# Kernel optimization log

Hardware: AMD Instinct MI355X
Metric: run time of the kernel (lower is better)

The kernel has to match this reference:

```python
import jax, jax.numpy as jnp
import numpy as np

FEAT_RES = 512
FEAT_DIM = 48
WIDTH = 128
IN_DIM = FEAT_DIM + 27 + 63  # 138
N_RAYS, N_SAMPLES = 4096, 128


def positional_encode(x, L):
    freqs = (2.0 ** jnp.arange(L)).astype(x.dtype)            # [L]
    xf = x[..., None, :] * freqs[:, None]                      # [..., L, 3]
    enc = jnp.concatenate([jnp.sin(xf), jnp.cos(xf)], axis=-1) # [..., L, 6]
    return jnp.concatenate([x, enc.reshape(x.shape[:-1] + (L * 6,))], axis=-1)


def grid_sample_bilinear(plane, gx, gy):
    # plane: [C, H, W]; gx, gy: [N, S] in [-1, 1]; align_corners=True, zeros padding
    H, W = plane.shape[-2], plane.shape[-1]
    ix = (gx + 1.0) * 0.5 * (W - 1)
    iy = (gy + 1.0) * 0.5 * (H - 1)
    x0 = jnp.floor(ix); y0 = jnp.floor(iy)
    x1 = x0 + 1.0;      y1 = y0 + 1.0
    wx1 = ix - x0; wx0 = 1.0 - wx1
    wy1 = iy - y0; wy0 = 1.0 - wy1

    def gather(xi, yi, w):
        valid = (xi >= 0) & (xi <= W - 1) & (yi >= 0) & (yi <= H - 1)
        xc = jnp.clip(xi, 0, W - 1).astype(jnp.int32)
        yc = jnp.clip(yi, 0, H - 1).astype(jnp.int32)
        v = plane[:, yc, xc]                                   # [C, N, S]
        return v * (w * valid.astype(w.dtype))[None]

    return (gather(x0, y0, wx0 * wy0) + gather(x1, y0, wx1 * wy0)
            + gather(x0, y1, wx0 * wy1) + gather(x1, y1, wx1 * wy1))


def setup_inputs() -> dict:
    key = jax.random.key(0)
    ks = jax.random.split(key, 12)
    x = jax.random.uniform(ks[0], (N_RAYS, N_SAMPLES, 3), jnp.float32, -3.0, 3.0)
    d = jax.random.normal(ks[1], (N_RAYS, 3), jnp.float32)
    d = d / jnp.linalg.norm(d, axis=-1, keepdims=True)
    feat = jax.random.normal(ks[2], (3, FEAT_DIM, FEAT_RES, FEAT_RES), jnp.float32)
    s = 0.05
    W0 = jax.random.normal(ks[3], (IN_DIM, WIDTH), jnp.float32) * s
    b0 = jnp.zeros((WIDTH,), jnp.float32)
    W1 = jax.random.normal(ks[4], (WIDTH, WIDTH), jnp.float32) * s
    b1 = jnp.zeros((WIDTH,), jnp.float32)
    W2 = jax.random.normal(ks[5], (WIDTH, WIDTH), jnp.float32) * s
    b2 = jnp.zeros((WIDTH,), jnp.float32)
    W3 = jax.random.normal(ks[6], (WIDTH, 4), jnp.float32) * s
    b3 = jnp.zeros((4,), jnp.float32)
    return {"x": x, "d": d, "feat": feat, "W0": W0, "b0": b0,
            "W1": W1, "b1": b1, "W2": W2, "b2": b2, "W3": W3, "b3": b3}


def reference(x, d, feat, W0, b0, W1, b1, W2, b2, W3, b3):
    x = x / 3.0                                                # [N, S, 3]
    f_xy = grid_sample_bilinear(feat[0], x[..., 0], x[..., 1])  # [C, N, S]
    f_yz = grid_sample_bilinear(feat[1], x[..., 1], x[..., 2])
    f_xz = grid_sample_bilinear(feat[2], x[..., 0], x[..., 2])
    f_sum = jnp.moveaxis(f_xy + f_yz + f_xz, 0, -1)            # [N, S, C]

    d_rep = jnp.broadcast_to(d[:, None, :], x.shape)           # [N, S, 3]
    h = jnp.concatenate([f_sum, positional_encode(d_rep, 4), positional_encode(x, 10)], axis=-1)

    h = jax.nn.relu(h @ W0 + b0)
    h = jax.nn.relu(h @ W1 + b1)
    h = jax.nn.relu(h @ W2 + b2)
    out = h @ W3 + b3                                          # [N, S, 4]
    return jnp.concatenate([out[..., :3], jax.nn.relu(out[..., 3:])], axis=-1)
```

## Files before the change

kernel.cpp:

```cpp
#include <hip/hip_runtime.h>
#include <hip/hip_bf16.h>
#include <cstdint>
#include <cstddef>

#define NPLANE 262144
#define HSTR 152
#define PW_LAYER 18432
#define NCELL 32768
#define NSAMP 524288

#define WS_FEAT_OFF 131072
#define FEAT_BYTES  75497472
#define WS_CNT_OFF  (WS_FEAT_OFF + FEAT_BYTES)
#define WS_OFFS_OFF (WS_CNT_OFF + 131072)
#define WS_XS_OFF   (WS_OFFS_OFF + 131072)
#define WS_END      (WS_XS_OFF + (size_t)NSAMP*16)

typedef unsigned int uint;
typedef __attribute__((ext_vector_type(16))) float f32x16;
typedef __attribute__((ext_vector_type(8))) short short8;

__device__ __forceinline__ float blo(uint u){ union{uint i; float f;} v; v.i = u<<16; return v.f; }
__device__ __forceinline__ float bhi(uint u){ union{uint i; float f;} v; v.i = u & 0xffff0000u; return v.f; }
__device__ __forceinline__ unsigned short bf16u(float f){
    __hip_bfloat16 h = __float2bfloat16(f);
    return *reinterpret_cast<unsigned short*>(&h);
}
__device__ __forceinline__ f32x16 mfma_(short8 a, short8 b, f32x16 c){
    return __builtin_amdgcn_mfma_f32_32x32x16_bf16(a, b, c, 0,0,0);
}

__device__ __forceinline__ uint part3(uint v){
    v &= 0x3ff;
    v = (v | (v<<16)) & 0x030000FFu;
    v = (v | (v<<8))  & 0x0300F00Fu;
    v = (v | (v<<4))  & 0x030C30C3u;
    v = (v | (v<<2))  & 0x09249249u;
    return v;
}
__device__ __forceinline__ uint cellkey(float x0, float x1, float x2){
    const float s = 1.0f/3.0f;
    const int cx = min(max((int)((x0*s+1.0f)*16.0f),0),31);
    const int cy = min(max((int)((x1*s+1.0f)*16.0f),0),31);
    const int cz = min(max((int)((x2*s+1.0f)*16.0f),0),31);
    return part3((uint)cx) | (part3((uint)cy)<<1) | (part3((uint)cz)<<2);
}

__global__ __launch_bounds__(256) void hist_k(const float* __restrict__ x, uint* __restrict__ counts){
    const int i = blockIdx.x*256 + threadIdx.x;
    if (i >= NSAMP) return;
    atomicAdd(&counts[cellkey(x[3*i], x[3*i+1], x[3*i+2])], 1u);
}

__global__ __launch_bounds__(1024) void scan_k(const uint* __restrict__ counts, uint* __restrict__ offs){
    __shared__ uint ps[1024];
    const int t = threadIdx.x;
    uint loc[32]; uint s = 0;
    #pragma unroll
    for (int i=0;i<32;++i){ loc[i] = counts[t*32+i]; s += loc[i]; }
    ps[t] = s; __syncthreads();
    for (int off=1; off<1024; off<<=1){
        uint v = (t>=off) ? ps[t-off] : 0u;
        __syncthreads();
        ps[t] += v;
        __syncthreads();
    }
    uint base = ps[t] - s;
    #pragma unroll
    for (int i=0;i<32;++i){ offs[t*32+i] = base; base += loc[i]; }
}

__global__ __launch_bounds__(256) void scatter_k(const float* __restrict__ x, uint* __restrict__ offs,
                                                 float4* __restrict__ xs){
    const int i = blockIdx.x*256 + threadIdx.x;
    if (i >= NSAMP) return;
    const float x0 = x[3*i], x1 = x[3*i+1], x2 = x[3*i+2];
    const uint pos = atomicAdd(&offs[cellkey(x0,x1,x2)], 1u);
    xs[pos] = make_float4(x0, x1, x2, __int_as_float(i));
}

__global__ __launch_bounds__(256) void prep_weights(const float* __restrict__ W0,
                                                    const float* __restrict__ W1,
                                                    const float* __restrict__ W2,
                                                    const float* __restrict__ b0,
                                                    const float* __restrict__ b1,
                                                    const float* __restrict__ b2,
                                                    unsigned short* __restrict__ ws){
    const int idx = blockIdx.x*256 + threadIdx.x;
    if (idx >= 3*PW_LAYER) return;
    const int L = idx / PW_LAYER, base = idx % PW_LAYER;
    const float* W = (L==0)? W0 : (L==1)? W1 : W2;
    const float* B = (L==0)? b0 : (L==1)? b1 : b2;
    const int KREAL = (L==0)? 138 : 128;
    const int e  = base & 7;
    const int l  = (base >> 3) & 63;
    const int fr = base >> 9;
    const int ks = fr >> 2, nt = fr & 3;
    const int k  = ks*16 + (l >> 5)*8 + e;
    const int n  = nt*32 + (l & 31);
    float v = 0.f;
    if (k < KREAL) v = W[k*128 + n];
    else if (k == KREAL) v = B[n];
    ws[idx] = bf16u(v);
}

__global__ __launch_bounds__(256) void transpose_feat_k(const float* __restrict__ feat,
                                                        unsigned short* __restrict__ featT){
    __shared__ unsigned short lb[256*50];
    const int tid = threadIdx.x;
    const int pos = blockIdx.x*256 + tid;
    const int p  = pos >> 18;
    const int yx = pos & (NPLANE-1);
    const float* src = feat + (size_t)p*48*NPLANE + yx;
    #pragma unroll 4
    for (int c = 0; c < 48; ++c){
        lb[tid*50 + c] = bf16u(src[(size_t)c*NPLANE]);
    }
    __syncthreads();
    uint4* dst = (uint4*)(featT + (size_t)blockIdx.x*(256*48));
    #pragma unroll
    for (int m = 0; m < 6; ++m){
        const int u4 = tid + m*256;
        const int byteoff = u4*16;
        const int smp = byteoff/96;
        const int off = (byteoff%96) >> 2;
        const uint* rw = (const uint*)(lb + smp*50);
        uint4 val; val.x = rw[off]; val.y = rw[off+1]; val.z = rw[off+2]; val.w = rw[off+3];
        dst[u4] = val;
    }
}

__device__ __forceinline__ void run_layer(unsigned short* H, const unsigned short* __restrict__ Wp,
                                          int lane, int ln31, int kg, const int* pr){
    const unsigned short* Hrow = H + ln31*HSTR;
    f32x16 acc[4];
    #pragma unroll
    for (int i=0;i<4;++i) acc[i] = (f32x16)0.f;
    #pragma unroll
    for (int h=0; h<2; ++h){
        short8 bf[10];
        #pragma unroll
        for (int i=0;i<10;++i){
            const int ks = i>>1, nt = 2*h + (i&1);
            bf[i] = *reinterpret_cast<const short8*>(Wp + (((ks*4+nt)*64 + lane) << 3));
        }
        #pragma unroll
        for (int ks=0; ks<5; ++ks){
            const short8 a = *reinterpret_cast<const short8*>(Hrow + ks*16 + kg*8);
            acc[2*h]   = mfma_(a, bf[2*ks],   acc[2*h]);
            acc[2*h+1] = mfma_(a, bf[2*ks+1], acc[2*h+1]);
        }
        #pragma unroll
        for (int i=0;i<8;++i){
            const int ks = 5 + (i>>1), nt = 2*h + (i&1);
            bf[i] = *reinterpret_cast<const short8*>(Wp + (((ks*4+nt)*64 + lane) << 3));
        }
        #pragma unroll
        for (int ks=5; ks<9; ++ks){
            const short8 a = *reinterpret_cast<const short8*>(Hrow + ks*16 + kg*8);
            acc[2*h]   = mfma_(a, bf[2*(ks-5)],   acc[2*h]);
            acc[2*h+1] = mfma_(a, bf[2*(ks-5)+1], acc[2*h+1]);
        }
    }
    #pragma unroll
    for (int nt=0;nt<4;++nt){
        #pragma unroll
        for (int r=0;r<16;++r){
            const int row = pr[r] >> 8;
            const int col = nt*32 + (pr[r] & 255);
            H[row*HSTR + col] = bf16u(fmaxf(acc[nt][r], 0.f));
        }
    }
}

template<int SORTED>
__global__ __launch_bounds__(64, 4) void nerf_mfma(
    const float* __restrict__ x, const float* __restrict__ d,
    const unsigned short* __restrict__ featT,
    const unsigned short* __restrict__ wp0, const unsigned short* __restrict__ wp1,
    const unsigned short* __restrict__ wp2,
    const float* __restrict__ W3, const float* __restrict__ b3,
    const float4* __restrict__ xs, float* __restrict__ out)
{
    __shared__ unsigned short H[32*HSTR];
    __shared__ uint sW3u[256];
    __shared__ float4 sX[32];

    const int lane = threadIdx.x;
    const int ln31 = lane & 31, kg = lane >> 5;
    int base;
    if (SORTED) base = (((int)blockIdx.x & 7)*2048 + ((int)blockIdx.x >> 3))*32;
    else        base = (int)blockIdx.x*32;

    short8 pa = {0,0,0,0,0,0,0,0}, pb = pa, qa = pa, qb = pa;
    if (kg == 0){
        pa[0] = (short)bf16u((float)ln31);
        pb[0] = (short)bf16u(1.0f);
        qa[0] = (short)bf16u(1.0f);
        qb[0] = (short)bf16u((float)ln31);
    }
    const f32x16 zz = (f32x16)0.f;
    const f32x16 D1 = __builtin_amdgcn_mfma_f32_32x32x16_bf16(pa, pb, zz, 0,0,0);
    const f32x16 D2 = __builtin_amdgcn_mfma_f32_32x32x16_bf16(qa, qb, zz, 0,0,0);
    int pr[16];
    #pragma unroll
    for (int r=0;r<16;++r) pr[r] = (((int)D1[r]) << 8) | (int)D2[r];

    if (lane < 32){
        if (SORTED) sX[lane] = xs[base + lane];
        else {
            const int g = base + lane;
            sX[lane] = make_float4(x[3*g], x[3*g+1], x[3*g+2], __int_as_float(g));
        }
    }

    #pragma unroll
    for (int j=0;j<4;++j){
        const int idx = lane*4 + j;
        const int k = idx >> 1, c = idx & 1;
        sW3u[idx] = ((uint)bf16u(W3[k*4 + 2*c])) | (((uint)bf16u(W3[k*4 + 2*c + 1])) << 16);
    }

    #pragma unroll
    for (int rr=0; rr<2; ++rr){
        if (rr == 1 && lane >= 32) break;
        const int s32 = rr ? lane : ln31;
        const int m   = rr ? 2 : kg;
        const float4 xr = sX[s32];
        const float xn = ((m==0)? xr.x : (m==1)? xr.y : xr.z) * (1.0f/3.0f);
        unsigned short* row = H + s32*HSTR;
        row[75+m] = bf16u(xn);
        float sv, cv;
        sincosf(xn, &sv, &cv);
        #pragma unroll
        for (int l=0;l<10;++l){
            row[78+l*6+m]   = bf16u(sv);
            row[78+l*6+3+m] = bf16u(cv);
            const float s2v = 2.0f*sv*cv;
            const float c2v = 1.0f - 2.0f*sv*sv;
            sv = s2v; cv = c2v;
        }
    }

    {
        const int s32 = lane >> 1, half = lane & 1;
        const int sid = __float_as_int(sX[s32].w);
        const int ray = sid >> 7;
        const float dv0 = d[ray*3], dv1 = d[ray*3+1], dv2 = d[ray*3+2];
        unsigned short* row = H + s32*HSTR;
        if (half == 0){
            row[48]=bf16u(dv0); row[49]=bf16u(dv1); row[50]=bf16u(dv2);
        }
        #pragma unroll
        for (int li=0; li<2; ++li){
            const int l = half*2 + li;
            const float sc = (float)(1<<l);
            float sv, cv;
            sincosf(dv0*sc, &sv, &cv); row[51+l*6+0]=bf16u(sv); row[54+l*6+0]=bf16u(cv);
            sincosf(dv1*sc, &sv, &cv); row[51+l*6+1]=bf16u(sv); row[54+l*6+1]=bf16u(cv);
            sincosf(dv2*sc, &sv, &cv); row[51+l*6+2]=bf16u(sv); row[54+l*6+2]=bf16u(cv);
        }
    }

    if (lane < 32){
        *(uint*)(H + lane*HSTR + 138)  = 0x00003f80u;
        *(uint2*)(H + lane*HSTR + 140) = make_uint2(0u, 0u);
    }

    #pragma unroll
    for (int rr=0; rr<3; ++rr){
        const int u = rr*64 + lane;
        const int s32 = u/6, ch = u - s32*6;
        const float4 xr = sX[s32];
        const float xn0 = xr.x*(1.0f/3.0f);
        const float xn1 = xr.y*(1.0f/3.0f);
        const float xn2 = xr.z*(1.0f/3.0f);
        const int c0 = ch*8;
        float acc[8];
        #pragma unroll
        for (int q=0;q<8;++q) acc[q]=0.f;
        #pragma unroll
        for (int p=0;p<3;++p){
            const float gx = (p==1)? xn1 : xn0;
            const float gy = (p==0)? xn1 : xn2;
            const float ix = ((gx+1.0f)*0.5f)*511.0f;
            const float iy = ((gy+1.0f)*0.5f)*511.0f;
            const float fx0 = floorf(ix), fy0 = floorf(iy);
            const float wx1 = ix - fx0, wy1 = iy - fy0;
            const float wx0 = 1.0f-wx1, wy0 = 1.0f-wy1;
            const int x0i = (int)fx0, y0i = (int)fy0;
            const int x0c = min(max(x0i,0),511),   x1c = min(max(x0i+1,0),511);
            const int y0c = min(max(y0i,0),511),   y1c = min(max(y0i+1,0),511);
            const uint r0 = (uint)(p*NPLANE + y0c*512);
            const uint r1 = (uint)(p*NPLANE + y1c*512);
            const uint  av[4] = {(r0+x0c)*48u, (r0+x1c)*48u, (r1+x0c)*48u, (r1+x1c)*48u};
            const float wv[4] = {wx0*wy0, wx1*wy0, wx0*wy1, wx1*wy1};
            #pragma unroll
            for (int cr=0;cr<4;++cr){
                const uint4 uv = *(const uint4*)(featT + av[cr] + c0);
                const float w = wv[cr];
                acc[0]+=w*blo(uv.x); acc[1]+=w*bhi(uv.x);
                acc[2]+=w*blo(uv.y); acc[3]+=w*bhi(uv.y);
                acc[4]+=w*blo(uv.z); acc[5]+=w*bhi(uv.z);
                acc[6]+=w*blo(uv.w); acc[7]+=w*bhi(uv.w);
            }
        }
        union { unsigned short us[8]; uint4 v; } pk;
        #pragma unroll
        for (int q=0;q<8;++q) pk.us[q] = bf16u(acc[q]);
        *(uint4*)(H + s32*HSTR + c0) = pk.v;
    }

    run_layer(H, wp0, lane, ln31, kg, pr);
    if (lane < 32) *(uint4*)(H + lane*HSTR + 128) = make_uint4(0x00003f80u,0u,0u,0u);
    else           *(uint4*)(H + ln31*HSTR + 136) = make_uint4(0u,0u,0u,0u);
    run_layer(H, wp1, lane, ln31, kg, pr);
    run_layer(H, wp2, lane, ln31, kg, pr);

    {
        const int s32 = lane >> 1, cp = lane & 1;
        const unsigned short* hrow = H + s32*HSTR;
        const int sid = __float_as_int(sX[s32].w);
        const float2 b3v = *(const float2*)(b3 + 2*cp);
        float a0 = b3v.x, a1 = b3v.y;
        #pragma unroll
        for (int q=0;q<16;++q){
            const uint4 u = *(const uint4*)(hrow + q*8);
            const int k = q*8;
            float h; uint wp_;
            h = blo(u.x); wp_ = sW3u[(k+0)*2+cp]; a0 += h*blo(wp_); a1 += h*bhi(wp_);
            h = bhi(u.x); wp_ = sW3u[(k+1)*2+cp]; a0 += h*blo(wp_); a1 += h*bhi(wp_);
            h = blo(u.y); wp_ = sW3u[(k+2)*2+cp]; a0 += h*blo(wp_); a1 += h*bhi(wp_);
            h = bhi(u.y); wp_ = sW3u[(k+3)*2+cp]; a0 += h*blo(wp_); a1 += h*bhi(wp_);
            h = blo(u.z); wp_ = sW3u[(k+4)*2+cp]; a0 += h*blo(wp_); a1 += h*bhi(wp_);
            h = bhi(u.z); wp_ = sW3u[(k+5)*2+cp]; a0 += h*blo(wp_); a1 += h*bhi(wp_);
            h = blo(u.w); wp_ = sW3u[(k+6)*2+cp]; a0 += h*blo(wp_); a1 += h*bhi(wp_);
            h = bhi(u.w); wp_ = sW3u[(k+7)*2+cp]; a0 += h*blo(wp_); a1 += h*bhi(wp_);
        }
        if (cp == 1) a1 = fmaxf(a1, 0.f);
        float2 o; o.x = a0; o.y = a1;
        *(float2*)(out + (size_t)sid*4 + 2*cp) = o;
    }
}

#define STR 148
#define SBLK 64
template<int K4, int KTAIL>
__device__ __forceinline__ void mlp_layer_fb(float (*Hs)[STR], const float* __restrict__ W,
                                             const float* __restrict__ B, int tid){
    const int tx = tid & 31, ty = tid >> 5;
    const int s0 = ty*8, j0 = tx*4;
    float acc[8][4];
    #pragma unroll
    for (int i=0;i<8;++i){ acc[i][0]=0.f; acc[i][1]=0.f; acc[i][2]=0.f; acc[i][3]=0.f; }
    for (int kk = 0; kk < K4; ++kk){
        const int k = kk*4;
        const float4 wa = *(const float4*)(W + (size_t)(k+0)*128 + j0);
        const float4 wb = *(const float4*)(W + (size_t)(k+1)*128 + j0);
        const float4 wc = *(const float4*)(W + (size_t)(k+2)*128 + j0);
        const float4 wd = *(const float4*)(W + (size_t)(k+3)*128 + j0);
        #pragma unroll
        for (int i=0;i<8;++i){
            const float4 h = *(const float4*)&Hs[s0+i][k];
            acc[i][0] += h.x*wa.x + h.y*wb.x + h.z*wc.x + h.w*wd.x;
            acc[i][1] += h.x*wa.y + h.y*wb.y + h.z*wc.y + h.w*wd.y;
            acc[i][2] += h.x*wa.z + h.y*wb.z + h.z*wc.z + h.w*wd.z;
            acc[i][3] += h.x*wa.w + h.y*wb.w + h.z*wc.w + h.w*wd.w;
        }
    }
    #pragma unroll
    for (int t=0;t<KTAIL;++t){
        const int k = K4*4+t;
        const float4 wa = *(const float4*)(W + (size_t)k*128 + j0);
        #pragma unroll
        for (int i=0;i<8;++i){
            const float h = Hs[s0+i][k];
            acc[i][0] += h*wa.x; acc[i][1] += h*wa.y; acc[i][2] += h*wa.z; acc[i][3] += h*wa.w;
        }
    }
    const float4 bb = *(const float4*)(B + j0);
    __syncthreads();
    #pragma unroll
    for (int i=0;i<8;++i){
        float4 o;
        o.x = fmaxf(acc[i][0]+bb.x, 0.f);
        o.y = fmaxf(acc[i][1]+bb.y, 0.f);
        o.z = fmaxf(acc[i][2]+bb.z, 0.f);
        o.w = fmaxf(acc[i][3]+bb.w, 0.f);
        *(float4*)&Hs[s0+i][j0] = o;
    }
    __syncthreads();
}

__global__ __launch_bounds__(256) void nerf_fused_fb(
    const float* __restrict__ x, const float* __restrict__ d,
    const float* __restrict__ feat,
    const float* __restrict__ W0, const float* __restrict__ b0,
    const float* __restrict__ W1, const float* __restrict__ b1,
    const float* __restrict__ W2, const float* __restrict__ b2,
    const float* __restrict__ W3, const float* __restrict__ b3,
    float* __restrict__ out)
{
    __shared__ float Hs[SBLK][STR];
    __shared__ uint4  sA[3][SBLK];
    __shared__ float4 sW[3][SBLK];

    const int tid = threadIdx.x;
    const int g0 = blockIdx.x * SBLK;

    if (tid < 192){
        const int s = tid & 63, p = tid >> 6;
        const int g = g0 + s;
        const float xn0 = x[3*g+0]/3.0f, xn1 = x[3*g+1]/3.0f, xn2 = x[3*g+2]/3.0f;
        const float gx = (p==1)? xn1 : xn0;
        const float gy = (p==0)? xn1 : xn2;
        const float ix = ((gx+1.0f)*0.5f)*511.0f;
        const float iy = ((gy+1.0f)*0.5f)*511.0f;
        const float fx0 = floorf(ix), fy0 = floorf(iy);
        const float wx1 = ix - fx0, wy1 = iy - fy0;
        const float wx0 = 1.0f-wx1, wy0 = 1.0f-wy1;
        const int x0i = (int)fx0, y0i = (int)fy0;
        const int x0c = min(max(x0i,0),511),   x1c = min(max(x0i+1,0),511);
        const int y0c = min(max(y0i,0),511),   y1c = min(max(y0i+1,0),511);
        const uint bp = (uint)p*48u*NPLANE;
        sA[p][s] = make_uint4(bp + y0c*512 + x0c, bp + y0c*512 + x1c,
                              bp + y1c*512 + x0c, bp + y1c*512 + x1c);
        sW[p][s] = make_float4(wx0*wy0, wx1*wy0, wx0*wy1, wx1*wy1);
    }
    if (tid < 64){
        const int s = tid, g = g0 + s;
        float xn[3];
        xn[0]=x[3*g+0]/3.0f; xn[1]=x[3*g+1]/3.0f; xn[2]=x[3*g+2]/3.0f;
        Hs[s][75]=xn[0]; Hs[s][76]=xn[1]; Hs[s][77]=xn[2];
        float f = 1.0f;
        for (int l=0;l<10;++l){
            #pragma unroll
            for (int m=0;m<3;++m){
                const float a = xn[m]*f;
                Hs[s][78+l*6+m]   = sinf(a);
                Hs[s][78+l*6+3+m] = cosf(a);
            }
            f *= 2.0f;
        }
    } else if (tid < 91){
        const int k = tid-64;
        const int ray = g0 >> 7;
        float v;
        if (k < 3) v = d[ray*3+k];
        else {
            const int l=(k-3)/6, r=(k-3)%6;
            const float a = d[ray*3 + (r%3)] * (float)(1<<l);
            v = (r<3)? sinf(a) : cosf(a);
        }
        for (int s2=0;s2<64;++s2) Hs[s2][48+k]=v;
    }
    __syncthreads();

    for (int it = tid; it < 384; it += 256){
        const int s = it & 63;
        const int c0 = (it >> 6)*8;
        float acc[8];
        #pragma unroll
        for (int q=0;q<8;++q) acc[q]=0.f;
        #pragma unroll
        for (int p=0;p<3;++p){
            const uint4  aa = sA[p][s];
            const float4 ww = sW[p][s];
            const uint  av[4] = {aa.x,aa.y,aa.z,aa.w};
            const float wv[4] = {ww.x,ww.y,ww.z,ww.w};
            #pragma unroll
            for (int cr=0;cr<4;++cr){
                const float w = wv[cr];
                const float* bsrc = feat + av[cr] + (size_t)c0*NPLANE;
                #pragma unroll
                for (int q=0;q<8;++q) acc[q] += w*bsrc[(size_t)q*NPLANE];
            }
        }
        *(float4*)&Hs[s][c0]   = make_float4(acc[0],acc[1],acc[2],acc[3]);
        *(float4*)&Hs[s][c0+4] = make_float4(acc[4],acc[5],acc[6],acc[7]);
    }
    __syncthreads();

    mlp_layer_fb<34,2>(Hs, W0, b0, tid);
    mlp_layer_fb<32,0>(Hs, W1, b1, tid);
    mlp_layer_fb<32,0>(Hs, W2, b2, tid);

    {
        const int s = tid>>2, j = tid&3;
        float acc = 0.f;
        for (int kk=0; kk<32; ++kk){
            const float4 h = *(const float4*)&Hs[s][kk*4];
            const int k = kk*4;
            acc += h.x*W3[(k+0)*4+j] + h.y*W3[(k+1)*4+j]
                 + h.z*W3[(k+2)*4+j] + h.w*W3[(k+3)*4+j];
        }
        acc += b3[j];
        if (j==3) acc = fmaxf(acc, 0.f);
        out[(size_t)blockIdx.x*256 + tid] = acc;
    }
}

extern "C" void kernel_launch(void* const* d_in, const int* in_sizes, int n_in,
                              void* d_out, int out_size, void* d_ws, size_t ws_size,
                              hipStream_t stream){
    (void)in_sizes; (void)n_in; (void)out_size;
    const float* x    = (const float*)d_in[0];
    const float* ddir = (const float*)d_in[1];
    const float* feat = (const float*)d_in[2];
    const float* W0 = (const float*)d_in[3];  const float* b0 = (const float*)d_in[4];
    const float* W1 = (const float*)d_in[5];  const float* b1 = (const float*)d_in[6];
    const float* W2 = (const float*)d_in[7];  const float* b2 = (const float*)d_in[8];
    const float* W3 = (const float*)d_in[9];  const float* b3 = (const float*)d_in[10];
    float* out = (float*)d_out;

    char* wsb = (char*)d_ws;
    unsigned short* wsu   = (unsigned short*)wsb;
    unsigned short* featT = (unsigned short*)(wsb + WS_FEAT_OFF);

    if (ws_size >= WS_END){
        uint*   counts = (uint*)(wsb + WS_CNT_OFF);
        uint*   offs   = (uint*)(wsb + WS_OFFS_OFF);
        float4* xsrec  = (float4*)(wsb + WS_XS_OFF);
        hipMemsetAsync(counts, 0, NCELL*sizeof(uint), stream);
        prep_weights<<<216, 256, 0, stream>>>(W0, W1, W2, b0, b1, b2, wsu);
        transpose_feat_k<<<3072, 256, 0, stream>>>(feat, featT);
        hist_k<<<2048, 256, 0, stream>>>(x, counts);
        scan_k<<<1, 1024, 0, stream>>>(counts, offs);
        scatter_k<<<2048, 256, 0, stream>>>(x, offs, xsrec);
        nerf_mfma<1><<<16384, 64, 0, stream>>>(x, ddir, featT,
                                               wsu, wsu + PW_LAYER, wsu + 2*PW_LAYER,
                                               W3, b3, xsrec, out);
    } else if (ws_size >= WS_CNT_OFF){
        prep_weights<<<216, 256, 0, stream>>>(W0, W1, W2, b0, b1, b2, wsu);
        transpose_feat_k<<<3072, 256, 0, stream>>>(feat, featT);
        nerf_mfma<0><<<16384, 64, 0, stream>>>(x, ddir, featT,
                                               wsu, wsu + PW_LAYER, wsu + 2*PW_LAYER,
                                               W3, b3, nullptr, out);
    } else {
        nerf_fused_fb<<<8192, 256, 0, stream>>>(x, ddir, feat,
                                                W0,b0,W1,b1,W2,b2,W3,b3, out);
    }
}
```

Before: 276.1 us.

## Switch to fp16 MFMA, fuse prep kernels, precompute ray encodings

```diff
diff --git a/kernel.cpp b/kernel.cpp
--- a/kernel.cpp
+++ b/kernel.cpp
@@ -1,5 +1,6 @@
 #include <hip/hip_runtime.h>
 #include <hip/hip_bf16.h>
+#include <hip/hip_fp16.h>
 #include <cstdint>
 #include <cstddef>
 
@@ -8,26 +9,31 @@
 #define PW_LAYER 18432
 #define NCELL 32768
 #define NSAMP 524288
+#define NRAY 4096
 
 #define WS_FEAT_OFF 131072
 #define FEAT_BYTES  75497472
 #define WS_CNT_OFF  (WS_FEAT_OFF + FEAT_BYTES)
 #define WS_OFFS_OFF (WS_CNT_OFF + 131072)
 #define WS_XS_OFF   (WS_OFFS_OFF + 131072)
-#define WS_END      (WS_XS_OFF + (size_t)NSAMP*16)
+#define WS_PED_OFF  (WS_XS_OFF + (size_t)NSAMP*16)
+#define WS_END      (WS_PED_OFF + (size_t)NRAY*28*2)
+
+#define TRS_BLKS 3072
+#define PREP_BLKS 216
+#define PED_BLKS 16
+#define K2_BLKS (1 + TRS_BLKS + PREP_BLKS + PED_BLKS)
 
 typedef unsigned int uint;
 typedef __attribute__((ext_vector_type(16))) float f32x16;
-typedef __attribute__((ext_vector_type(8))) short short8;
-
-__device__ __forceinline__ float blo(uint u){ union{uint i; float f;} v; v.i = u<<16; return v.f; }
-__device__ __forceinline__ float bhi(uint u){ union{uint i; float f;} v; v.i = u & 0xffff0000u; return v.f; }
-__device__ __forceinline__ unsigned short bf16u(float f){
-    __hip_bfloat16 h = __float2bfloat16(f);
+typedef _Float16 half8 __attribute__((ext_vector_type(8)));
+
+__device__ __forceinline__ unsigned short f16u(float f){
+    __half h = __float2half(f);
     return *reinterpret_cast<unsigned short*>(&h);
 }
-__device__ __forceinline__ f32x16 mfma_(short8 a, short8 b, f32x16 c){
-    return __builtin_amdgcn_mfma_f32_32x32x16_bf16(a, b, c, 0,0,0);
+__device__ __forceinline__ f32x16 mfma16_(half8 a, half8 b, f32x16 c){
+    return __builtin_amdgcn_mfma_f32_32x32x16_f16(a, b, c, 0,0,0);
 }
 
 __device__ __forceinline__ uint part3(uint v){
@@ -52,22 +58,94 @@
     atomicAdd(&counts[cellkey(x[3*i], x[3*i+1], x[3*i+2])], 1u);
 }
 
-__global__ __launch_bounds__(1024) void scan_k(const uint* __restrict__ counts, uint* __restrict__ offs){
-    __shared__ uint ps[1024];
-    const int t = threadIdx.x;
-    uint loc[32]; uint s = 0;
-    #pragma unroll
-    for (int i=0;i<32;++i){ loc[i] = counts[t*32+i]; s += loc[i]; }
-    ps[t] = s; __syncthreads();
-    for (int off=1; off<1024; off<<=1){
-        uint v = (t>=off) ? ps[t-off] : 0u;
+__global__ __launch_bounds__(256) void prepass_k(const float* __restrict__ feat,
+                                                 const float* __restrict__ W0,
+                                                 const float* __restrict__ W1,
+                                                 const float* __restrict__ W2,
+                                                 const float* __restrict__ b0,
+                                                 const float* __restrict__ b1,
+                                                 const float* __restrict__ b2,
+                                                 const float* __restrict__ d,
+                                                 const uint* __restrict__ counts,
+                                                 uint* __restrict__ offs,
+                                                 unsigned short* __restrict__ featT,
+                                                 unsigned short* __restrict__ wp,
+                                                 unsigned short* __restrict__ ped){
+    const int bid = blockIdx.x, tid = threadIdx.x;
+    if (bid == 0){
+        __shared__ uint ps[256];
+        uint s = 0;
+        for (int i=0;i<128;++i) s += counts[tid*128+i];
+        ps[tid] = s; __syncthreads();
+        for (int off=1; off<256; off<<=1){
+            uint v = (tid>=off) ? ps[tid-off] : 0u;
+            __syncthreads();
+            ps[tid] += v;
+            __syncthreads();
+        }
+        uint base = ps[tid] - s;
+        for (int i=0;i<128;++i){ uint c = counts[tid*128+i]; offs[tid*128+i] = base; base += c; }
+        return;
+    }
+    if (bid <= TRS_BLKS){
+        __shared__ unsigned short lb[256*50];
+        const int pos = (bid-1)*256 + tid;
+        const int p  = pos >> 18;
+        const int yx = pos & (NPLANE-1);
+        const float* src = feat + (size_t)p*48*NPLANE + yx;
+        #pragma unroll 4
+        for (int c = 0; c < 48; ++c){
+            lb[tid*50 + c] = f16u(src[(size_t)c*NPLANE]);
+        }
         __syncthreads();
-        ps[t] += v;
-        __syncthreads();
-    }
-    uint base = ps[t] - s;
-    #pragma unroll
-    for (int i=0;i<32;++i){ offs[t*32+i] = base; base += loc[i]; }
+        uint4* dst = (uint4*)(featT + (size_t)(bid-1)*(256*48));
+        #pragma unroll
+        for (int m = 0; m < 6; ++m){
+            const int u4 = tid + m*256;
+            const int byteoff = u4*16;
+            const int smp = byteoff/96;
+            const int off = (byteoff%96) >> 2;
+            const uint* rw = (const uint*)(lb + smp*50);
+            uint4 val; val.x = rw[off]; val.y = rw[off+1]; val.z = rw[off+2]; val.w = rw[off+3];
+            dst[u4] = val;
+        }
+        return;
+    }
+    if (bid <= TRS_BLKS + PREP_BLKS){
+        const int idx = (bid - 1 - TRS_BLKS)*256 + tid;
+        if (idx >= 3*PW_LAYER) return;
+        const int L = idx / PW_LAYER, base = idx % PW_LAYER;
+        const float* W = (L==0)? W0 : (L==1)? W1 : W2;
+        const float* B = (L==0)? b0 : (L==1)? b1 : b2;
+        const int KREAL = (L==0)? 138 : 128;
+        const int e  = base & 7;
+        const int l  = (base >> 3) & 63;
+        const int fr = base >> 9;
+        const int ks = fr >> 2, nt = fr & 3;
+        const int k  = ks*16 + (l >> 5)*8 + e;
+        const int n  = nt*32 + (l & 31);
+        float v = 0.f;
+        if (k < KREAL) v = W[k*128 + n];
+        else if (k == KREAL) v = B[n];
+        wp[idx] = f16u(v);
+        return;
+    }
+    {
+        const int ray = (bid - 1 - TRS_BLKS - PREP_BLKS)*256 + tid;
+        if (ray >= NRAY) return;
+        const float dv0 = d[ray*3], dv1 = d[ray*3+1], dv2 = d[ray*3+2];
+        unsigned short* row = ped + ray*28;
+        row[0]=f16u(dv0); row[1]=f16u(dv1); row[2]=f16u(dv2);
+        #pragma unroll
+        for (int l=0;l<4;++l){
+            const float sc = (float)(1<<l);
+            float sv, cv;
+            __sincosf(dv0*sc, &sv, &cv); row[3+l*6+0]=f16u(sv); row[3+l*6+3]=f16u(cv);
+            __sincosf(dv1*sc, &sv, &cv); row[3+l*6+1]=f16u(sv); row[3+l*6+4]=f16u(cv);
+            __sincosf(dv2*sc, &sv, &cv); row[3+l*6+2]=f16u(sv); row[3+l*6+5]=f16u(cv);
+        }
+        row[27] = 0;
+    }
 }
 
 __global__ __launch_bounds__(256) void scatter_k(const float* __restrict__ x, uint* __restrict__ offs,
@@ -79,57 +157,6 @@
     xs[pos] = make_float4(x0, x1, x2, __int_as_float(i));
 }
 
-__global__ __launch_bounds__(256) void prep_weights(const float* __restrict__ W0,
-                                                    const float* __restrict__ W1,
-                                                    const float* __restrict__ W2,
-                                                    const float* __restrict__ b0,
-                                                    const float* __restrict__ b1,
-                                                    const float* __restrict__ b2,
-                                                    unsigned short* __restrict__ ws){
-    const int idx = blockIdx.x*256 + threadIdx.x;
-    if (idx >= 3*PW_LAYER) return;
-    const int L = idx / PW_LAYER, base = idx % PW_LAYER;
-    const float* W = (L==0)? W0 : (L==1)? W1 : W2;
-    const float* B = (L==0)? b0 : (L==1)? b1 : b2;
-    const int KREAL = (L==0)? 138 : 128;
-    const int e  = base & 7;
-    const int l  = (base >> 3) & 63;
-    const int fr = base >> 9;
-    const int ks = fr >> 2, nt = fr & 3;
-    const int k  = ks*16 + (l >> 5)*8 + e;
-    const int n  = nt*32 + (l & 31);
-    float v = 0.f;
-    if (k < KREAL) v = W[k*128 + n];
-    else if (k == KREAL) v = B[n];
-    ws[idx] = bf16u(v);
-}
-
-__global__ __launch_bounds__(256) void transpose_feat_k(const float* __restrict__ feat,
-                                                        unsigned short* __restrict__ featT){
-    __shared__ unsigned short lb[256*50];
-    const int tid = threadIdx.x;
-    const int pos = blockIdx.x*256 + tid;
-    const int p  = pos >> 18;
-    const int yx = pos & (NPLANE-1);
-    const float* src = feat + (size_t)p*48*NPLANE + yx;
-    #pragma unroll 4
-    for (int c = 0; c < 48; ++c){
-        lb[tid*50 + c] = bf16u(src[(size_t)c*NPLANE]);
-    }
-    __syncthreads();
-    uint4* dst = (uint4*)(featT + (size_t)blockIdx.x*(256*48));
-    #pragma unroll
-    for (int m = 0; m < 6; ++m){
-        const int u4 = tid + m*256;
-        const int byteoff = u4*16;
-        const int smp = byteoff/96;
-        const int off = (byteoff%96) >> 2;
-        const uint* rw = (const uint*)(lb + smp*50);
-        uint4 val; val.x = rw[off]; val.y = rw[off+1]; val.z = rw[off+2]; val.w = rw[off+3];
-        dst[u4] = val;
-    }
-}
-
 __device__ __forceinline__ void run_layer(unsigned short* H, const unsigned short* __restrict__ Wp,
                                           int lane, int ln31, int kg, const int* pr){
     const unsigned short* Hrow = H + ln31*HSTR;
@@ -138,28 +165,28 @@
     for (int i=0;i<4;++i) acc[i] = (f32x16)0.f;
     #pragma unroll
     for (int h=0; h<2; ++h){
-        short8 bf[10];
+        half8 bf[10];
         #pragma unroll
         for (int i=0;i<10;++i){
             const int ks = i>>1, nt = 2*h + (i&1);
-            bf[i] = *reinterpret_cast<const short8*>(Wp + (((ks*4+nt)*64 + lane) << 3));
+            bf[i] = *reinterpret_cast<const half8*>(Wp + (((ks*4+nt)*64 + lane) << 3));
         }
         #pragma unroll
         for (int ks=0; ks<5; ++ks){
-            const short8 a = *reinterpret_cast<const short8*>(Hrow + ks*16 + kg*8);
-            acc[2*h]   = mfma_(a, bf[2*ks],   acc[2*h]);
-            acc[2*h+1] = mfma_(a, bf[2*ks+1], acc[2*h+1]);
+            const half8 a = *reinterpret_cast<const half8*>(Hrow + ks*16 + kg*8);
+            acc[2*h]   = mfma16_(a, bf[2*ks],   acc[2*h]);
+            acc[2*h+1] = mfma16_(a, bf[2*ks+1], acc[2*h+1]);
         }
         #pragma unroll
         for (int i=0;i<8;++i){
             const int ks = 5 + (i>>1), nt = 2*h + (i&1);
-            bf[i] = *reinterpret_cast<const short8*>(Wp + (((ks*4+nt)*64 + lane) << 3));
+            bf[i] = *reinterpret_cast<const half8*>(Wp + (((ks*4+nt)*64 + lane) << 3));
         }
         #pragma unroll
         for (int ks=5; ks<9; ++ks){
-            const short8 a = *reinterpret_cast<const short8*>(Hrow + ks*16 + kg*8);
-            acc[2*h]   = mfma_(a, bf[2*(ks-5)],   acc[2*h]);
-            acc[2*h+1] = mfma_(a, bf[2*(ks-5)+1], acc[2*h+1]);
+            const half8 a = *reinterpret_cast<const half8*>(Hrow + ks*16 + kg*8);
+            acc[2*h]   = mfma16_(a, bf[2*(ks-5)],   acc[2*h]);
+            acc[2*h+1] = mfma16_(a, bf[2*(ks-5)+1], acc[2*h+1]);
         }
     }
     #pragma unroll
@@ -168,58 +195,43 @@
         for (int r=0;r<16;++r){
             const int row = pr[r] >> 8;
             const int col = nt*32 + (pr[r] & 255);
-            H[row*HSTR + col] = bf16u(fmaxf(acc[nt][r], 0.f));
-        }
-    }
-}
-
-template<int SORTED>
+            H[row*HSTR + col] = f16u(fmaxf(acc[nt][r], 0.f));
+        }
+    }
+}
+
 __global__ __launch_bounds__(64, 4) void nerf_mfma(
-    const float* __restrict__ x, const float* __restrict__ d,
     const unsigned short* __restrict__ featT,
     const unsigned short* __restrict__ wp0, const unsigned short* __restrict__ wp1,
     const unsigned short* __restrict__ wp2,
     const float* __restrict__ W3, const float* __restrict__ b3,
-    const float4* __restrict__ xs, float* __restrict__ out)
+    const float4* __restrict__ xs, const unsigned short* __restrict__ ped,
+    float* __restrict__ out)
 {
     __shared__ unsigned short H[32*HSTR];
-    __shared__ uint sW3u[256];
+    __shared__ float sW3[516];
     __shared__ float4 sX[32];
 
     const int lane = threadIdx.x;
     const int ln31 = lane & 31, kg = lane >> 5;
-    int base;
-    if (SORTED) base = (((int)blockIdx.x & 7)*2048 + ((int)blockIdx.x >> 3))*32;
-    else        base = (int)blockIdx.x*32;
-
-    short8 pa = {0,0,0,0,0,0,0,0}, pb = pa, qa = pa, qb = pa;
+    const int base = (((int)blockIdx.x & 7)*2048 + ((int)blockIdx.x >> 3))*32;
+
+    half8 pa = (half8)0, pb = (half8)0, qa = (half8)0, qb = (half8)0;
     if (kg == 0){
-        pa[0] = (short)bf16u((float)ln31);
-        pb[0] = (short)bf16u(1.0f);
-        qa[0] = (short)bf16u(1.0f);
-        qb[0] = (short)bf16u((float)ln31);
+        pa[0] = (_Float16)(float)ln31;
+        pb[0] = (_Float16)1.0f;
+        qa[0] = (_Float16)1.0f;
+        qb[0] = (_Float16)(float)ln31;
     }
     const f32x16 zz = (f32x16)0.f;
-    const f32x16 D1 = __builtin_amdgcn_mfma_f32_32x32x16_bf16(pa, pb, zz, 0,0,0);
-    const f32x16 D2 = __builtin_amdgcn_mfma_f32_32x32x16_bf16(qa, qb, zz, 0,0,0);
+    const f32x16 D1 = mfma16_(pa, pb, zz);
+    const f32x16 D2 = mfma16_(qa, qb, zz);
     int pr[16];
     #pragma unroll
     for (int r=0;r<16;++r) pr[r] = (((int)D1[r]) << 8) | (int)D2[r];
 
-    if (lane < 32){
-        if (SORTED) sX[lane] = xs[base + lane];
-        else {
-            const int g = base + lane;
-            sX[lane] = make_float4(x[3*g], x[3*g+1], x[3*g+2], __int_as_float(g));
-        }
-    }
-
-    #pragma unroll
-    for (int j=0;j<4;++j){
-        const int idx = lane*4 + j;
-        const int k = idx >> 1, c = idx & 1;
-        sW3u[idx] = ((uint)bf16u(W3[k*4 + 2*c])) | (((uint)bf16u(W3[k*4 + 2*c + 1])) << 16);
-    }
+    if (lane < 32) sX[lane] = xs[base + lane];
+    for (int i = lane; i < 516; i += 64) sW3[i] = (i < 512) ? W3[i] : b3[i-512];
 
     #pragma unroll
     for (int rr=0; rr<2; ++rr){
@@ -229,13 +241,13 @@
         const float4 xr = sX[s32];
         const float xn = ((m==0)? xr.x : (m==1)? xr.y : xr.z) * (1.0f/3.0f);
         unsigned short* row = H + s32*HSTR;
-        row[75+m] = bf16u(xn);
+        row[75+m] = f16u(xn);
         float sv, cv;
-        sincosf(xn, &sv, &cv);
+        __sincosf(xn, &sv, &cv);
         #pragma unroll
         for (int l=0;l<10;++l){
-            row[78+l*6+m]   = bf16u(sv);
-            row[78+l*6+3+m] = bf16u(cv);
+            row[78+l*6+m]   = f16u(sv);
+            row[78+l*6+3+m] = f16u(cv);
             const float s2v = 2.0f*sv*cv;
             const float c2v = 1.0f - 2.0f*sv*sv;
             sv = s2v; cv = c2v;
@@ -245,25 +257,20 @@
     {
         const int s32 = lane >> 1, half = lane & 1;
         const int sid = __float_as_int(sX[s32].w);
-        const int ray = sid >> 7;
-        const float dv0 = d[ray*3], dv1 = d[ray*3+1], dv2 = d[ray*3+2];
-        unsigned short* row = H + s32*HSTR;
+        const uint* src = (const uint*)(ped + (sid >> 7)*28) + half*7;
+        uint* dstu = (uint*)(H + s32*HSTR + 48) + half*7;
         if (half == 0){
-            row[48]=bf16u(dv0); row[49]=bf16u(dv1); row[50]=bf16u(dv2);
-        }
-        #pragma unroll
-        for (int li=0; li<2; ++li){
-            const int l = half*2 + li;
-            const float sc = (float)(1<<l);
-            float sv, cv;
-            sincosf(dv0*sc, &sv, &cv); row[51+l*6+0]=bf16u(sv); row[54+l*6+0]=bf16u(cv);
-            sincosf(dv1*sc, &sv, &cv); row[51+l*6+1]=bf16u(sv); row[54+l*6+1]=bf16u(cv);
-            sincosf(dv2*sc, &sv, &cv); row[51+l*6+2]=bf16u(sv); row[54+l*6+2]=bf16u(cv);
+            #pragma unroll
+            for (int i=0;i<7;++i) dstu[i] = src[i];
+        } else {
+            #pragma unroll
+            for (int i=0;i<6;++i) dstu[i] = src[i];
+            H[s32*HSTR + 74] = ((const unsigned short*)src)[12];
         }
     }
 
     if (lane < 32){
-        *(uint*)(H + lane*HSTR + 138)  = 0x00003f80u;
+        *(uint*)(H + lane*HSTR + 138)  = 0x00003C00u;
         *(uint2*)(H + lane*HSTR + 140) = make_uint2(0u, 0u);
     }
 
@@ -276,9 +283,9 @@
         const float xn1 = xr.y*(1.0f/3.0f);
         const float xn2 = xr.z*(1.0f/3.0f);
         const int c0 = ch*8;
-        float acc[8];
-        #pragma unroll
-        for (int q=0;q<8;++q) acc[q]=0.f;
+        __half2 acc[4];
+        #pragma unroll
+        for (int q=0;q<4;++q) acc[q] = __float2half2_rn(0.f);
         #pragma unroll
         for (int p=0;p<3;++p){
             const float gx = (p==1)? xn1 : xn0;
@@ -298,21 +305,22 @@
             #pragma unroll
             for (int cr=0;cr<4;++cr){
                 const uint4 uv = *(const uint4*)(featT + av[cr] + c0);
-                const float w = wv[cr];
-                acc[0]+=w*blo(uv.x); acc[1]+=w*bhi(uv.x);
-                acc[2]+=w*blo(uv.y); acc[3]+=w*bhi(uv.y);
-                acc[4]+=w*blo(uv.z); acc[5]+=w*bhi(uv.z);
-                acc[6]+=w*blo(uv.w); acc[7]+=w*bhi(uv.w);
+                const __half2 w2 = __float2half2_rn(wv[cr]);
+                union { uint4 v; __half2 h[4]; } t; t.v = uv;
+                acc[0] = __hfma2(t.h[0], w2, acc[0]);
+                acc[1] = __hfma2(t.h[1], w2, acc[1]);
+                acc[2] = __hfma2(t.h[2], w2, acc[2]);
+                acc[3] = __hfma2(t.h[3], w2, acc[3]);
             }
         }
-        union { unsigned short us[8]; uint4 v; } pk;
-        #pragma unroll
-        for (int q=0;q<8;++q) pk.us[q] = bf16u(acc[q]);
+        union { __half2 h[4]; uint4 v; } pk;
+        #pragma unroll
+        for (int q=0;q<4;++q) pk.h[q] = acc[q];
         *(uint4*)(H + s32*HSTR + c0) = pk.v;
     }
 
     run_layer(H, wp0, lane, ln31, kg, pr);
-    if (lane < 32) *(uint4*)(H + lane*HSTR + 128) = make_uint4(0x00003f80u,0u,0u,0u);
+    if (lane < 32) *(uint4*)(H + lane*HSTR + 128) = make_uint4(0x00003C00u,0u,0u,0u);
     else           *(uint4*)(H + ln31*HSTR + 136) = make_uint4(0u,0u,0u,0u);
     run_layer(H, wp1, lane, ln31, kg, pr);
     run_layer(H, wp2, lane, ln31, kg, pr);
@@ -321,30 +329,30 @@
         const int s32 = lane >> 1, cp = lane & 1;
         const unsigned short* hrow = H + s32*HSTR;
         const int sid = __float_as_int(sX[s32].w);
-        const float2 b3v = *(const float2*)(b3 + 2*cp);
-        float a0 = b3v.x, a1 = b3v.y;
+        const int jp = 2*cp;
+        float a0 = sW3[512+jp], a1 = sW3[513+jp];
         #pragma unroll
         for (int q=0;q<16;++q){
-            const uint4 u = *(const uint4*)(hrow + q*8);
+            union { uint4 v; __half2 h[4]; } u;
+            u.v = *(const uint4*)(hrow + q*8);
             const int k = q*8;
-            float h; uint wp_;
-            h = blo(u.x); wp_ = sW3u[(k+0)*2+cp]; a0 += h*blo(wp_); a1 += h*bhi(wp_);
-            h = bhi(u.x); wp_ = sW3u[(k+1)*2+cp]; a0 += h*blo(wp_); a1 += h*bhi(wp_);
-            h = blo(u.y); wp_ = sW3u[(k+2)*2+cp]; a0 += h*blo(wp_); a1 += h*bhi(wp_);
-            h = bhi(u.y); wp_ = sW3u[(k+3)*2+cp]; a0 += h*blo(wp_); a1 += h*bhi(wp_);
-            h = blo(u.z); wp_ = sW3u[(k+4)*2+cp]; a0 += h*blo(wp_); a1 += h*bhi(wp_);
-            h = bhi(u.z); wp_ = sW3u[(k+5)*2+cp]; a0 += h*blo(wp_); a1 += h*bhi(wp_);
-            h = blo(u.w); wp_ = sW3u[(k+6)*2+cp]; a0 += h*blo(wp_); a1 += h*bhi(wp_);
-            h = bhi(u.w); wp_ = sW3u[(k+7)*2+cp]; a0 += h*blo(wp_); a1 += h*bhi(wp_);
+            #pragma unroll
+            for (int j2=0;j2<4;++j2){
+                const float2 f = __half22float2(u.h[j2]);
+                const int k2 = k + j2*2;
+                a0 += f.x*sW3[(k2+0)*4+jp] + f.y*sW3[(k2+1)*4+jp];
+                a1 += f.x*sW3[(k2+0)*4+jp+1] + f.y*sW3[(k2+1)*4+jp+1];
+            }
         }
         if (cp == 1) a1 = fmaxf(a1, 0.f);
         float2 o; o.x = a0; o.y = a1;
-        *(float2*)(out + (size_t)sid*4 + 2*cp) = o;
+        *(float2*)(out + (size_t)sid*4 + jp) = o;
     }
 }
 
 #define STR 148
 #define SBLK 64
+typedef unsigned int uint;
 template<int K4, int KTAIL>
 __device__ __forceinline__ void mlp_layer_fb(float (*Hs)[STR], const float* __restrict__ W,
                                              const float* __restrict__ B, int tid){
@@ -514,28 +522,22 @@
     float* out = (float*)d_out;
 
     char* wsb = (char*)d_ws;
-    unsigned short* wsu   = (unsigned short*)wsb;
-    unsigned short* featT = (unsigned short*)(wsb + WS_FEAT_OFF);
 
     if (ws_size >= WS_END){
+        unsigned short* wsu   = (unsigned short*)wsb;
+        unsigned short* featT = (unsigned short*)(wsb + WS_FEAT_OFF);
         uint*   counts = (uint*)(wsb + WS_CNT_OFF);
         uint*   offs   = (uint*)(wsb + WS_OFFS_OFF);
         float4* xsrec  = (float4*)(wsb + WS_XS_OFF);
+        unsigned short* ped = (unsigned short*)(wsb + WS_PED_OFF);
         hipMemsetAsync(counts, 0, NCELL*sizeof(uint), stream);
-        prep_weights<<<216, 256, 0, stream>>>(W0, W1, W2, b0, b1, b2, wsu);
-        transpose_feat_k<<<3072, 256, 0, stream>>>(feat, featT);
         hist_k<<<2048, 256, 0, stream>>>(x, counts);
-        scan_k<<<1, 1024, 0, stream>>>(counts, offs);
+        prepass_k<<<K2_BLKS, 256, 0, stream>>>(feat, W0, W1, W2, b0, b1, b2, ddir,
+                                               counts, offs, featT, wsu, ped);
         scatter_k<<<2048, 256, 0, stream>>>(x, offs, xsrec);
-        nerf_mfma<1><<<16384, 64, 0, stream>>>(x, ddir, featT,
-                                               wsu, wsu + PW_LAYER, wsu + 2*PW_LAYER,
-                                               W3, b3, xsrec, out);
-    } else if (ws_size >= WS_CNT_OFF){
-        prep_weights<<<216, 256, 0, stream>>>(W0, W1, W2, b0, b1, b2, wsu);
-        transpose_feat_k<<<3072, 256, 0, stream>>>(feat, featT);
-        nerf_mfma<0><<<16384, 64, 0, stream>>>(x, ddir, featT,
-                                               wsu, wsu + PW_LAYER, wsu + 2*PW_LAYER,
-                                               W3, b3, nullptr, out);
+        nerf_mfma<<<16384, 64, 0, stream>>>(featT,
+                                            wsu, wsu + PW_LAYER, wsu + 2*PW_LAYER,
+                                            W3, b3, xsrec, ped, out);
     } else {
         nerf_fused_fb<<<8192, 256, 0, stream>>>(x, ddir, feat,
                                                 W0,b0,W1,b1,W2,b2,W3,b3, out);
```

New measurement: 303.7 us. 1.1x slower.
